# Kernel tuning notes

Hardware: AMD Instinct MI355X
Metric: run time of the kernel (lower is better)

The kernel has to match this reference:

```python
import jax, jax.numpy as jnp
import numpy as np

NUM_GRAPHS = 1024
NODES_PER_GRAPH = 128
NUM_EDGES = 1048576
D_IN = 128          # n_heads * head_out_feats = input/concat dim
ATT_HEADS = 2       # intra/inter GATConv(d, 32, 2) as in HDN-DDI repo
ATT_OUT = 32
POOL_HEADS = 2      # pool = GATConv(128, 64, 2)
POOL_OUT = 64
EPS = 1e-5          # PyG LayerNorm eps


def _segment_softmax(e, seg, n):
    # numerically-stable softmax over edges grouped by destination node
    m = jax.ops.segment_max(e, seg, num_segments=n)
    m = jnp.where(jnp.isfinite(m), m, 0.0)
    p = jnp.exp(e - m[seg])
    s = jax.ops.segment_sum(p, seg, num_segments=n)
    return p / (s[seg] + 1e-16)


def _gat(x_src, x_dst, edge_index, w_src, w_dst, att_src, att_dst, bias, self_loops):
    # PyG GATConv: linear -> per-head attention logits -> leaky_relu(0.2) ->
    # softmax over incoming edges -> weighted sum of source features -> concat heads + bias
    H, C = att_src.shape
    nd = x_dst.shape[0]
    hs = (x_src @ w_src).reshape(-1, H, C)   # [Ns,H,C]
    hd = (x_dst @ w_dst).reshape(-1, H, C)   # [Nd,H,C]
    a_s = jnp.einsum('nhc,hc->nh', hs, att_src)
    a_d = jnp.einsum('nhc,hc->nh', hd, att_dst)
    src, dst = edge_index[0], edge_index[1]
    if self_loops:  # PyG default add_self_loops=True (non-bipartite case)
        loop = jnp.arange(nd)
        src = jnp.concatenate([src, loop])
        dst = jnp.concatenate([dst, loop])
    e = jax.nn.leaky_relu(a_s[src] + a_d[dst], 0.2)  # [E,H]
    alpha = _segment_softmax(e, dst, nd)
    out = jax.ops.segment_sum(hs[src] * alpha[:, :, None], dst, num_segments=nd)
    return out.reshape(nd, H * C) + bias


def _graph_layernorm(x, batch, weight, bias, n_graphs):
    # PyG LayerNorm(mode='graph'): normalize over all nodes+channels of each graph
    f = x.shape[-1]
    cnt = jax.ops.segment_sum(jnp.ones((x.shape[0],), x.dtype), batch, num_segments=n_graphs)
    norm = jnp.maximum(cnt, 1.0) * f
    mean = jax.ops.segment_sum(x.sum(-1), batch, num_segments=n_graphs) / norm
    xc = x - mean[batch][:, None]
    var = jax.ops.segment_sum((xc * xc).sum(-1), batch, num_segments=n_graphs) / norm
    return (xc / jnp.sqrt(var + EPS)[batch][:, None]) * weight + bias


def setup_inputs() -> dict:
    key = jax.random.key(0)
    ks = jax.random.split(key, 24)
    B, P, E, D = NUM_GRAPHS, NODES_PER_GRAPH, NUM_EDGES, D_IN
    N = B * P

    def intra_edges(k):  # within-graph edges, no self-loops
        k1, k2, k3 = jax.random.split(k, 3)
        g = jax.random.randint(k1, (E,), 0, B)
        s = jax.random.randint(k2, (E,), 0, P)
        d = (s + 1 + jax.random.randint(k3, (E,), 0, P - 1)) % P
        return jnp.stack([g * P + s, g * P + d])

    def inter_edges(k):  # bipartite head-node -> tail-node edges within same graph pair
        k1, k2, k3 = jax.random.split(k, 3)
        g = jax.random.randint(k1, (E,), 0, B)
        s = jax.random.randint(k2, (E,), 0, P)
        d = jax.random.randint(k3, (E,), 0, P)
        return jnp.stack([g * P + s, g * P + d])

    batch = jnp.repeat(jnp.arange(B), P)
    # one global supernode (type 2) per graph: the last node
    y = jnp.tile(jnp.concatenate([jnp.zeros((P - 1,), jnp.int32), jnp.array([2], jnp.int32)]), B)
    p = lambda k, shape: jax.random.normal(k, shape, jnp.float32) * 0.1
    return {
        'h_x': jax.random.normal(ks[0], (N, D), jnp.float32),
        't_x': jax.random.normal(ks[1], (N, D), jnp.float32),
        'h_edge_index': intra_edges(ks[2]),
        't_edge_index': intra_edges(ks[3]),
        'b_edge_index': inter_edges(ks[4]),
        'h_batch': batch,
        't_batch': batch,
        'h_y': y,
        't_y': y,
        'w_intra': p(ks[5], (D, ATT_HEADS * ATT_OUT)),
        'att_intra_src': p(ks[6], (ATT_HEADS, ATT_OUT)),
        'att_intra_dst': p(ks[7], (ATT_HEADS, ATT_OUT)),
        'b_intra': jnp.zeros((ATT_HEADS * ATT_OUT,), jnp.float32),
        'w_inter_src': p(ks[8], (D, ATT_HEADS * ATT_OUT)),
        'w_inter_dst': p(ks[9], (D, ATT_HEADS * ATT_OUT)),
        'att_inter_src': p(ks[10], (ATT_HEADS, ATT_OUT)),
        'att_inter_dst': p(ks[11], (ATT_HEADS, ATT_OUT)),
        'b_inter': jnp.zeros((ATT_HEADS * ATT_OUT,), jnp.float32),
        'w_pool': p(ks[12], (D, POOL_HEADS * POOL_OUT)),
        'att_pool_src': p(ks[13], (POOL_HEADS, POOL_OUT)),
        'att_pool_dst': p(ks[14], (POOL_HEADS, POOL_OUT)),
        'b_pool': jnp.zeros((POOL_HEADS * POOL_OUT,), jnp.float32),
        'ln_weight': jnp.ones((D,), jnp.float32),
        'ln_bias': jnp.zeros((D,), jnp.float32),
    }


def reference(h_x, t_x, h_edge_index, t_edge_index, b_edge_index, h_batch, t_batch, h_y, t_y,
              w_intra, att_intra_src, att_intra_dst, b_intra,
              w_inter_src, w_inter_dst, att_inter_src, att_inter_dst, b_inter,
              w_pool, att_pool_src, att_pool_dst, b_pool, ln_weight, ln_bias):
    h_in = jax.nn.elu(h_x)
    t_in = jax.nn.elu(t_x)
    # intra-graph attention (shared GATConv applied to both drug graphs)
    h_intra = _gat(h_in, h_in, h_edge_index, w_intra, w_intra, att_intra_src, att_intra_dst, b_intra, True)
    t_intra = _gat(t_in, t_in, t_edge_index, w_intra, w_intra, att_intra_src, att_intra_dst, b_intra, True)
    # inter-graph (bipartite) attention: h->t and reversed t->h with shared weights
    t_inter = _gat(h_in, t_in, b_edge_index, w_inter_src, w_inter_dst, att_inter_src, att_inter_dst, b_inter, False)
    h_inter = _gat(t_in, h_in, b_edge_index[::-1], w_inter_src, w_inter_dst, att_inter_src, att_inter_dst, b_inter, False)
    h_rep = jnp.concatenate([h_intra, h_inter], 1)  # [N, 128]
    t_rep = jnp.concatenate([t_intra, t_inter], 1)
    h_nx = jax.nn.elu(_graph_layernorm(h_rep, h_batch, ln_weight, ln_bias, NUM_GRAPHS))
    t_nx = jax.nn.elu(_graph_layernorm(t_rep, t_batch, ln_weight, ln_bias, NUM_GRAPHS))
    h_out = _gat(h_nx, h_nx, h_edge_index, w_pool, w_pool, att_pool_src, att_pool_dst, b_pool, True)
    t_out = _gat(t_nx, t_nx, t_edge_index, w_pool, w_pool, att_pool_src, att_pool_dst, b_pool, True)
    # get_node: gather the single type-2 supernode per graph (exactly NUM_GRAPHS of them)
    h_idx = jnp.where(h_y == 2, size=NUM_GRAPHS)[0]
    t_idx = jnp.where(t_y == 2, size=NUM_GRAPHS)[0]
    return h_out, t_out, h_out[h_idx], t_out[t_idx]
```

## Files before the change

### kernel.cpp

```cpp
#include <hip/hip_runtime.h>
#include <hip/hip_bf16.h>

#define NN 131072
#define NG 1024
#define NE 1048576
#define EB 16384
#define NB 64
#define EMAX 1536

typedef __hip_bfloat16 bf16;
typedef __attribute__((ext_vector_type(8))) short short8v;
typedef __attribute__((ext_vector_type(4))) float f32x4;

__device__ __forceinline__ float b2f(bf16 v){ return __bfloat162float(v); }
__device__ __forceinline__ bf16 f2b(float v){ return __float2bfloat16(v); }
__device__ __forceinline__ unsigned short f2bu(float v){ bf16 b = f2b(v); return *(unsigned short*)&b; }
__device__ __forceinline__ float eluf(float x){ return x > 0.f ? x : expm1f(x); }
__device__ __forceinline__ float lrelu(float x){ return x >= 0.f ? x : 0.2f*x; }

__device__ __forceinline__ float ldx(const void* p, size_t i, int f){
  return f ? ((const float*)p)[i] : b2f(((const bf16*)p)[i]);
}

struct EPtrs { const int *s0,*d0,*s1,*d1,*s2,*d2,*s3,*d3; };

__global__ void detect_dtype(const unsigned short* __restrict__ x, int* __restrict__ flag){
  if (blockIdx.x==0 && threadIdx.x==0){
    int bad = 0;
    for (int i=0;i<2048;i++){
      unsigned short e = (x[i] >> 7) & 0xFF;
      if (e == 0xFF) bad++;
      else if (e >= 0x90) bad++;
      else if (e != 0 && e < 0x60) bad++;
    }
    *flag = (bad > 64) ? 1 : 0;
  }
}

__global__ __launch_bounds__(256) void hist_bagg(EPtrs ep, int* __restrict__ Hb){
  __shared__ int cnt[NG];
  int set = blockIdx.y, blk = blockIdx.x, t = threadIdx.x;
  const int* dp = set==0 ? ep.d0 : set==1 ? ep.d1 : set==2 ? ep.d2 : ep.d3;
  for (int i=t;i<NG;i+=256) cnt[i]=0;
  __syncthreads();
  int e0 = blk*EB;
  for (int i=t;i<EB;i+=256) atomicAdd(&cnt[dp[e0+i]>>7],1);
  __syncthreads();
  for (int i=t;i<NG;i+=256) Hb[((size_t)set*NB+blk)*NG+i] = cnt[i];
}

__global__ __launch_bounds__(1024) void scan_bagg(const int* __restrict__ Hb, int* __restrict__ Bb,
                                                  int* __restrict__ base_gs){
  __shared__ int sh[1024];
  int set = blockIdx.x, t = threadIdx.x;
  int run = 0;
  for (int b=0;b<NB;b++){
    int v = Hb[((size_t)set*NB + b)*NG + t];
    Bb[((size_t)set*NB + b)*NG + t] = run;
    run += v;
  }
  int val = run; sh[t] = run; __syncthreads();
  for (int d=1; d<1024; d<<=1){
    int add = (t>=d)? sh[t-d] : 0; __syncthreads();
    val += add; sh[t] = val; __syncthreads();
  }
  int binbase = val - run;
  base_gs[set*(NG+1) + t] = binbase;
  if (t==1023) base_gs[set*(NG+1)+NG] = val;
  for (int b=0;b<NB;b++) Bb[((size_t)set*NB + b)*NG + t] += binbase;
}

__global__ __launch_bounds__(256) void scatter_bagg(EPtrs ep, const int* __restrict__ Bb,
                                                    unsigned short* __restrict__ pk){
  __shared__ int cur[NG];
  int set = blockIdx.y, blk = blockIdx.x, t = threadIdx.x;
  const int* sp = set==0 ? ep.s0 : set==1 ? ep.s1 : set==2 ? ep.s2 : ep.s3;
  const int* dp = set==0 ? ep.d0 : set==1 ? ep.d1 : set==2 ? ep.d2 : ep.d3;
  for (int i=t;i<NG;i+=256) cur[i] = Bb[((size_t)set*NB+blk)*NG+i];
  __syncthreads();
  int e0 = blk*EB;
  for (int i=t;i<EB;i+=256){
    int e = e0+i;
    int d = dp[e], s = sp[e];
    int p = atomicAdd(&cur[d>>7],1);
    pk[(size_t)set*NE + p] = (unsigned short)(((d & 127) << 8) | (s & 127));
  }
}

__global__ __launch_bounds__(256) void build_csr(const unsigned short* __restrict__ pk, const int* __restrict__ base,
                                                 unsigned char* __restrict__ srcs8, int* __restrict__ offs4){
  __shared__ int hist[128], excl[128], cur[128];
  __shared__ unsigned char ob[8192];
  int set = blockIdx.y, g = blockIdx.x, t = threadIdx.x;
  int n0 = base[set*(NG+1) + g], n1 = base[set*(NG+1) + g + 1];
  int cnt = min(n1 - n0, 8192);
  if (t < 128) hist[t] = 0;
  __syncthreads();
  const unsigned short* PK = pk + (size_t)set*NE + n0;
  for (int i=t; i<cnt; i+=256) atomicAdd(&hist[PK[i]>>8], 1);
  __syncthreads();
  if (t < 128) excl[t] = hist[t];
  __syncthreads();
  for (int d=1; d<128; d<<=1){
    int v = (t < 128 && t >= d) ? excl[t-d] : 0;
    __syncthreads();
    if (t < 128) excl[t] += v;
    __syncthreads();
  }
  if (t < 128){
    int e_ = excl[t] - hist[t];
    cur[t] = e_;
    offs4[(size_t)set*(NN+1) + g*128 + t] = n0 + e_;
  }
  if (g == NG-1 && t == 0) offs4[(size_t)set*(NN+1) + NN] = NE;
  __syncthreads();
  for (int i=t; i<cnt; i+=256){
    unsigned short v = PK[i];
    int p = atomicAdd(&cur[v>>8], 1);
    ob[p] = (unsigned char)(v & 127);
  }
  __syncthreads();
  unsigned char* S = srcs8 + (size_t)set*NE + n0;
  for (int i=t; i<cnt; i+=256) S[i] = ob[i];
}

__global__ __launch_bounds__(256) void prep_kernel(
    const void* w_intra, const void* w_isrc, const void* w_idst, const void* att_xd, const void* w_pool,
    const void* att_is, const void* att_id, const void* att_xs,
    const void* att_ps, const void* att_pd,
    const void* b_intra, const void* b_inter, const void* b_pool,
    const void* ln_w, const void* ln_b,
    bf16* __restrict__ Wtc, bf16* __restrict__ Wtp, float* __restrict__ vdst, float* __restrict__ sm,
    const int* __restrict__ fp){
  int f = *fp;
  int t = threadIdx.x;
  for (int i=t; i<16384; i+=256){
    int j = i & 7, l = (i>>3) & 63, ks = (i>>9) & 3, nt = i >> 11;
    int k = ks*32 + ((l>>4)<<3) + j;
    int c = nt*16 + (l & 15);
    float w1 = (c < 64) ? ldx(w_intra, k*64 + c, f) : ldx(w_isrc, k*64 + (c-64), f);
    Wtc[i] = f2b(w1);
    Wtp[i] = f2b(ldx(w_pool, k*128 + c, f));
  }
  {
    int k = t>>1, h = t&1; float a = 0.f;
    for (int c=0;c<32;c++) a += ldx(w_idst, k*64 + h*32 + c, f) * ldx(att_xd, h*32 + c, f);
    vdst[t] = a;
  }
  if (t < 64){
    sm[t]     = ldx(att_is, t, f);
    sm[64+t]  = ldx(att_id, t, f);
    sm[128+t] = ldx(att_xs, t, f);
    sm[448+t] = ldx(b_intra, t, f);
    sm[512+t] = ldx(b_inter, t, f);
  }
  if (t < 128){
    sm[192+t] = ldx(att_ps, t, f);
    sm[320+t] = ldx(att_pd, t, f);
    sm[576+t] = ldx(b_pool, t, f);
    sm[704+t] = ldx(ln_w, t, f);
    sm[832+t] = ldx(ln_b, t, f);
  }
}

template<int MODE>
__global__ __launch_bounds__(256) void gemm_fused(const void* A, const bf16* __restrict__ Wt, bf16* __restrict__ C,
    const int* __restrict__ fp, const int* __restrict__ fsel, size_t aoff_bf, size_t aoff_f32,
    const float* __restrict__ vdst,
    const float* __restrict__ attA, const float* __restrict__ attB, const float* __restrict__ attC,
    float* __restrict__ oS, float* __restrict__ oD, float* __restrict__ oX, float* __restrict__ oDx){
  constexpr bool ELU = (MODE==0);
  const bf16* Ab = (const bf16*)A + ((fp == nullptr && fsel && *fsel) ? aoff_f32 : aoff_bf);
  int tid = threadIdx.x;
  int w = tid >> 6, l = tid & 63;
  int lr = l & 15, lg = l >> 4;
  size_t row = (size_t)blockIdx.x*64 + w*16 + lr;
  int f = fp ? *fp : 0;
  f32x4 acc[8];
  #pragma unroll
  for (int nt=0;nt<8;nt++) acc[nt] = (f32x4){0.f,0.f,0.f,0.f};
  float dx0 = 0.f, dx1 = 0.f;
  #pragma unroll
  for (int ks=0;ks<4;ks++){
    short8v af;
    size_t ab = row*128 + ks*32 + lg*8;
    if (fp){
      if (f){
        const float* Af = (const float*)A;
        #pragma unroll
        for (int j=0;j<8;j++){
          float v = Af[ab+j]; if (ELU) v = eluf(v);
          if constexpr (MODE==0){ int k = ks*32+lg*8+j; dx0 += v*vdst[k*2]; dx1 += v*vdst[k*2+1]; }
          ((unsigned short*)&af)[j] = f2bu(v);
        }
      } else {
        const unsigned short* Au = (const unsigned short*)A;
        short8v raw = *(const short8v*)(Au + ab);
        #pragma unroll
        for (int j=0;j<8;j++){
          bf16 b; *(unsigned short*)&b = ((unsigned short*)&raw)[j];
          float v = b2f(b); if (ELU) v = eluf(v);
          if constexpr (MODE==0){ int k = ks*32+lg*8+j; dx0 += v*vdst[k*2]; dx1 += v*vdst[k*2+1]; }
          ((unsigned short*)&af)[j] = f2bu(v);
        }
      }
    } else {
      af = *(const short8v*)((const unsigned short*)Ab + ab);
    }
    #pragma unroll
    for (int nt=0;nt<8;nt++){
      short8v bfr = *(const short8v*)((const unsigned short*)Wt + (size_t)((nt*4+ks)*64 + l)*8);
      acc[nt] = __builtin_amdgcn_mfma_f32_16x16x32_bf16(af, bfr, acc[nt], 0, 0, 0);
    }
  }
  if constexpr (MODE==0){
    dx0 += __shfl_xor(dx0, 16); dx0 += __shfl_xor(dx0, 32);
    dx1 += __shfl_xor(dx1, 16); dx1 += __shfl_xor(dx1, 32);
    if (lg == 0){ oDx[row*2] = dx0; oDx[row*2+1] = dx1; }
  }
  size_t crow = (size_t)blockIdx.x*64 + w*16 + lg*4;
  #pragma unroll
  for (int nt=0;nt<8;nt++)
    #pragma unroll
    for (int r=0;r<4;r++)
      C[(crow + r)*128 + nt*16 + lr] = f2b(acc[nt][r]);
  #pragma unroll
  for (int rg=0; rg<4; ++rg){
    float pS0=0.f,pS1=0.f,pD0=0.f,pD1=0.f,pX0=0.f,pX1=0.f;
    #pragma unroll
    for (int nt=0;nt<8;nt++){
      float v = acc[nt][rg];
      int c = nt*16 + lr;
      if constexpr (MODE==0){
        if (nt<4){
          float a=attA[c], b=attB[c];
          if (nt<2){ pS0+=v*a; pD0+=v*b; } else { pS1+=v*a; pD1+=v*b; }
        } else {
          float xw=attC[c-64];
          if (nt<6) pX0+=v*xw; else pX1+=v*xw;
        }
      } else {
        float a=attA[c], b=attB[c];
        if (nt<4){ pS0+=v*a; pD0+=v*b; } else { pS1+=v*a; pD1+=v*b; }
      }
    }
    #pragma unroll
    for (int o=1;o<16;o<<=1){
      pS0+=__shfl_xor(pS0,o); pS1+=__shfl_xor(pS1,o);
      pD0+=__shfl_xor(pD0,o); pD1+=__shfl_xor(pD1,o);
      if constexpr (MODE==0){ pX0+=__shfl_xor(pX0,o); pX1+=__shfl_xor(pX1,o); }
    }
    if (lr == 0){
      size_t n = crow + rg;
      oS[n*2]=pS0; oS[n*2+1]=pS1;
      oD[n*2]=pD0; oD[n*2+1]=pD1;
      if constexpr (MODE==0){ oX[n*2]=pX0; oX[n*2+1]=pX1; }
    }
  }
}

struct GatSet {
  const int* offs;
  const unsigned char* srcs;
  const bf16* F;
  const float* aS;
  const float* aD;
  const float* bias;
  int col_in;
  int self_loops;
  int col_off;
  int pad;
  size_t obase_bf, obase_f32, gbase;
};
struct GatSet4 { GatSet s[4]; };

template<int FD>
__global__ __launch_bounds__(512) void gat_mfma(GatSet4 sets, void* out,
    const int* __restrict__ fp, const int* __restrict__ fsel){
  constexpr int NH = FD/2;
  constexpr int NT = NH/16;
  constexpr int KSH = (FD==64)?5:6;
  __shared__ bf16 Ft[NH*136];
  __shared__ bf16 Pm[128*136];
  __shared__ float2 aSs[128];
  __shared__ float rsum[128];
  __shared__ unsigned char ss[EMAX];
  __shared__ int begs[129];
  const GatSet S = sets.s[blockIdx.y];
  int fo = fp ? *fp : -1;
  size_t obase = (fsel && *fsel) ? S.obase_f32 : S.obase_bf;
  int g = blockIdx.x, t = threadIdx.x;

  if (t < 129) begs[t] = S.offs[g*128 + t];
  if (t >= 256 && t < 384) aSs[t-256] = ((const float2*)S.aS)[g*128 + (t-256)];
  __syncthreads();
  int gbeg = begs[0];
  int Eg = min(begs[128] - gbeg, EMAX);
  int w = t >> 6, l = t & 63, lr = l & 15, lg = l >> 4;

  #pragma unroll
  for (int h=0; h<2; ++h){
    for (int i=t; i<128*68; i+=512) ((unsigned int*)Pm)[i] = 0;
    if (h==0) for (int i=t; i<Eg; i+=512) ss[i] = S.srcs[gbeg + i];
    __syncthreads();
    if (t < 128){
      int r = t;
      float ad = S.aD[(size_t)(g*128+r)*2 + h];
      int b = begs[r]-gbeg, e = min(begs[r+1]-gbeg, EMAX);
      float rs = 0.f;
      unsigned short* Pr = (unsigned short*)Pm + r*136;
      for (int j=b; j<e; ++j){
        int s = ss[j];
        float2 as2 = aSs[s];
        float p = __expf(lrelu((h ? as2.y : as2.x) + ad));
        bf16 ov; *(unsigned short*)&ov = Pr[s];
        Pr[s] = f2bu(b2f(ov) + p);
        rs += p;
      }
      if (S.self_loops){
        float2 as2 = aSs[r];
        float p = __expf(lrelu((h ? as2.y : as2.x) + ad));
        bf16 ov; *(unsigned short*)&ov = Pr[r];
        Pr[r] = f2bu(b2f(ov) + p);
        rs += p;
      }
      rsum[r] = rs;
    } else {
      const unsigned short* Fu = (const unsigned short*)S.F;
      unsigned short* FtU = (unsigned short*)Ft;
      int ft = t - 128;
      for (int i=ft; i<NH*128; i+=384){
        int c = i & (NH-1), k = i >> KSH;
        FtU[c*136 + k] = Fu[((size_t)(g*128+k))*128 + S.col_in + h*NH + c];
      }
    }
    __syncthreads();
    f32x4 acc[NT];
    #pragma unroll
    for (int nt=0;nt<NT;nt++) acc[nt] = (f32x4){0.f,0.f,0.f,0.f};
    #pragma unroll
    for (int ks=0;ks<4;ks++){
      short8v af = *(const short8v*)((const unsigned short*)Pm + (w*16+lr)*136 + ks*32 + lg*8);
      #pragma unroll
      for (int nt=0;nt<NT;nt++){
        short8v bfr = *(const short8v*)((const unsigned short*)Ft + (nt*16 + lr)*136 + ks*32 + lg*8);
        acc[nt] = __builtin_amdgcn_mfma_f32_16x16x32_bf16(af, bfr, acc[nt], 0, 0, 0);
      }
    }
    #pragma unroll
    for (int rg=0; rg<4; ++rg){
      int rrow = w*16 + lg*4 + rg;
      float rinv = 1.f / (rsum[rrow] + 1e-16f);
      int n = g*128 + rrow;
      bool gw = (fp != nullptr) && (rrow == 127);
      #pragma unroll
      for (int nt=0;nt<NT;nt++){
        int c = h*NH + nt*16 + lr;
        float o = acc[nt][rg]*rinv + S.bias[c];
        size_t oi = obase + (size_t)n*128 + S.col_off + c;
        if (fo > 0){
          ((float*)out)[oi] = o;
          if (gw) ((float*)out)[S.gbase + (size_t)g*128 + c] = o;
        } else {
          ((bf16*)out)[oi] = f2b(o);
          if (gw) ((bf16*)out)[S.gbase + (size_t)g*128 + c] = f2b(o);
        }
      }
    }
    __syncthreads();
  }
}

__global__ __launch_bounds__(512) void graph_ln_m(bf16* R_, size_t off_t_bf, size_t off_t_f32,
    const int* __restrict__ fsel, const float* __restrict__ wv, const float* __restrict__ bv){
  __shared__ float sh1[8], sh2[8];
  int g = blockIdx.x, t = threadIdx.x;
  int side = g >> 10, gl = g & 1023;
  size_t soff = side ? ((*fsel) ? off_t_f32 : off_t_bf) : 0;
  unsigned short* Ru = (unsigned short*)(R_ + soff + (size_t)gl*16384);
  short8v v[4];
  #pragma unroll
  for (int q=0;q<4;q++) v[q] = *(short8v*)(Ru + q*4096 + t*8);
  float s1=0.f, s2=0.f;
  #pragma unroll
  for (int q=0;q<4;q++)
    #pragma unroll
    for (int j=0;j<8;j++){
      bf16 b; *(unsigned short*)&b = ((unsigned short*)&v[q])[j];
      float x = b2f(b); s1 += x; s2 += x*x;
    }
  #pragma unroll
  for (int o=32;o;o>>=1){ s1 += __shfl_xor(s1,o); s2 += __shfl_xor(s2,o); }
  if ((t&63)==0){ sh1[t>>6]=s1; sh2[t>>6]=s2; }
  __syncthreads();
  float S1=0.f,S2=0.f;
  #pragma unroll
  for (int i=0;i<8;i++){ S1+=sh1[i]; S2+=sh2[i]; }
  float mean = S1 * (1.f/16384.f);
  float var = fmaxf(S2*(1.f/16384.f) - mean*mean, 0.f);
  float rstd = rsqrtf(var + 1e-5f);
  #pragma unroll
  for (int q=0;q<4;q++){
    short8v ov;
    #pragma unroll
    for (int j=0;j<8;j++){
      int c = (t*8 + j) & 127;
      bf16 b; *(unsigned short*)&b = ((unsigned short*)&v[q])[j];
      float y = (b2f(b)-mean)*rstd*wv[c] + bv[c];
      ((unsigned short*)&ov)[j] = f2bu(y>0.f ? y : expm1f(y));
    }
    *(short8v*)(Ru + q*4096 + t*8) = ov;
  }
}

extern "C" void kernel_launch(void* const* d_in, const int* in_sizes, int n_in,
                              void* d_out, int out_size, void* d_ws, size_t ws_size,
                              hipStream_t stream){
  (void)in_sizes; (void)n_in; (void)out_size; (void)ws_size;
  const void* h_x = d_in[0];
  const void* t_x = d_in[1];
  const int* h_ei = (const int*)d_in[2];
  const int* t_ei = (const int*)d_in[3];
  const int* b_ei = (const int*)d_in[4];

  char* base = (char*)d_ws;
  size_t off = 0;
  auto alloc = [&](size_t bytes)->char*{ char* p = base + off; off += (bytes + 255) & ~(size_t)255; return p; };
  bf16* AB_h     = (bf16*)alloc((size_t)NN*128*2);
  bf16* AB_t     = (bf16*)alloc((size_t)NN*128*2);
  unsigned short* pk = (unsigned short*)alloc((size_t)4*NE*2);
  unsigned char* srcs8 = (unsigned char*)alloc((size_t)4*NE);
  int* offs4     = (int*)alloc((size_t)4*(NN+1)*4);
  int* Hb        = (int*)alloc((size_t)4*NB*NG*4);
  int* Bb        = (int*)alloc((size_t)4*NB*NG*4);
  int* base_gs   = (int*)alloc((size_t)4*(NG+1)*4);
  float* aSi_h   = (float*)alloc((size_t)NN*2*4);
  float* aDi_h   = (float*)alloc((size_t)NN*2*4);
  float* aSx_h   = (float*)alloc((size_t)NN*2*4);
  float* aSi_t   = (float*)alloc((size_t)NN*2*4);
  float* aDi_t   = (float*)alloc((size_t)NN*2*4);
  float* aSx_t   = (float*)alloc((size_t)NN*2*4);
  float* aDx_h   = (float*)alloc((size_t)NN*2*4);
  float* aDx_t   = (float*)alloc((size_t)NN*2*4);
  bf16* Wtc      = (bf16*)alloc(16384*2);
  bf16* Wtp      = (bf16*)alloc(16384*2);
  float* vdst    = (float*)alloc(256*4);
  float* sm      = (float*)alloc(960*4);
  int* flag      = (int*)alloc(256);

  const size_t REPT_BF = (size_t)NN*128, REPT_F32 = (size_t)2*NN*128;

  detect_dtype<<<1,64,0,stream>>>((const unsigned short*)h_x, flag);

  EPtrs ep;
  ep.s0 = h_ei;      ep.d0 = h_ei + NE;
  ep.s1 = t_ei;      ep.d1 = t_ei + NE;
  ep.s2 = b_ei;      ep.d2 = b_ei + NE;
  ep.s3 = b_ei + NE; ep.d3 = b_ei;
  hist_bagg<<<dim3(NB,4),256,0,stream>>>(ep, Hb);
  scan_bagg<<<4,1024,0,stream>>>(Hb, Bb, base_gs);
  scatter_bagg<<<dim3(NB,4),256,0,stream>>>(ep, Bb, pk);
  build_csr<<<dim3(NG,4),256,0,stream>>>(pk, base_gs, srcs8, offs4);

  prep_kernel<<<1,256,0,stream>>>(d_in[9], d_in[13], d_in[14], d_in[16], d_in[18],
      d_in[10], d_in[11], d_in[15], d_in[19], d_in[20],
      d_in[12], d_in[17], d_in[21], d_in[22], d_in[23],
      Wtc, Wtp, vdst, sm, flag);

  const int* offs_h = offs4;
  const int* offs_t = offs4 + (NN+1);
  const int* offs_ht= offs4 + 2*(NN+1);
  const int* offs_th= offs4 + 3*(NN+1);
  const unsigned char* srcs_h = srcs8;
  const unsigned char* srcs_t = srcs8 + NE;
  const unsigned char* srcs_ht= srcs8 + (size_t)2*NE;
  const unsigned char* srcs_th= srcs8 + (size_t)3*NE;

  gemm_fused<0><<<2048,256,0,stream>>>(h_x, Wtc, AB_h, flag, nullptr, 0, 0,
      vdst, sm+0, sm+64, sm+128, aSi_h, aDi_h, aSx_h, aDx_h);
  gemm_fused<0><<<2048,256,0,stream>>>(t_x, Wtc, AB_t, flag, nullptr, 0, 0,
      vdst, sm+0, sm+64, sm+128, aSi_t, aDi_t, aSx_t, aDx_t);

  {
    GatSet4 L;
    L.s[0] = { offs_h,  srcs_h,  AB_h, aSi_h, aDi_h, sm+448, 0,  1, 0,  0, 0,        0,         0 };
    L.s[1] = { offs_t,  srcs_t,  AB_t, aSi_t, aDi_t, sm+448, 0,  1, 0,  0, REPT_BF,  REPT_F32,  0 };
    L.s[2] = { offs_ht, srcs_ht, AB_h, aSx_h, aDx_t, sm+512, 64, 0, 64, 0, REPT_BF,  REPT_F32,  0 };
    L.s[3] = { offs_th, srcs_th, AB_t, aSx_t, aDx_h, sm+512, 64, 0, 64, 0, 0,        0,         0 };
    gat_mfma<64><<<dim3(NG,4),512,0,stream>>>(L, d_out, nullptr, flag);
  }

  graph_ln_m<<<2048,512,0,stream>>>((bf16*)d_out, REPT_BF, REPT_F32, flag, sm+704, sm+832);

  gemm_fused<1><<<2048,256,0,stream>>>(d_out, Wtp, AB_h, nullptr, flag, 0, 0,
      nullptr, sm+192, sm+320, nullptr, aSi_h, aDi_h, nullptr, nullptr);
  gemm_fused<1><<<2048,256,0,stream>>>(d_out, Wtp, AB_t, nullptr, flag, REPT_BF, REPT_F32,
      nullptr, sm+192, sm+320, nullptr, aSi_t, aDi_t, nullptr, nullptr);

  {
    size_t gb_h = (size_t)2*NN*128;
    size_t gb_t = gb_h + (size_t)NG*128;
    GatSet4 P;
    P.s[0] = { offs_h, srcs_h, AB_h, aSi_h, aDi_h, sm+576, 0, 1, 0, 0, 0,              0,              gb_h };
    P.s[1] = { offs_t, srcs_t, AB_t, aSi_t, aDi_t, sm+576, 0, 1, 0, 0, (size_t)NN*128, (size_t)NN*128, gb_t };
    P.s[2] = P.s[0]; P.s[3] = P.s[0];
    gat_mfma<128><<<dim3(NG,2),512,0,stream>>>(P, d_out, flag, flag);
  }
}
```

Measured before the change: 615.5 us.

## Replace per-graph CSR build with in-block packed edge multiplicity matrix

Drops the build_csr kernel and instead has each GAT block scatter packed (dst,src) edges into a shared-memory 128x128 matrix of 4-bit multiplicity counters via atomics. Attention weights are then computed densely for all 128 sources per row by four threads in parallel, instead of one thread serially walking each row's edge list. Shared tiles switch from padding to XOR swizzling, and the feature tile load is no longer overlapped with the softmax pass. This removes one kernel launch and its global memory traffic, plus the serial per-row loop, at the cost of dense exp work and a risk of counter overflow for highly duplicated edges.

```diff
diff --git a/kernel.cpp b/kernel.cpp
--- a/kernel.cpp
+++ b/kernel.cpp
@@ -6,7 +6,6 @@
 #define NE 1048576
 #define EB 16384
 #define NB 64
-#define EMAX 1536
 
 typedef __hip_bfloat16 bf16;
 typedef __attribute__((ext_vector_type(8))) short short8v;
@@ -85,43 +84,6 @@
     int p = atomicAdd(&cur[d>>7],1);
     pk[(size_t)set*NE + p] = (unsigned short)(((d & 127) << 8) | (s & 127));
   }
-}
-
-__global__ __launch_bounds__(256) void build_csr(const unsigned short* __restrict__ pk, const int* __restrict__ base,
-                                                 unsigned char* __restrict__ srcs8, int* __restrict__ offs4){
-  __shared__ int hist[128], excl[128], cur[128];
-  __shared__ unsigned char ob[8192];
-  int set = blockIdx.y, g = blockIdx.x, t = threadIdx.x;
-  int n0 = base[set*(NG+1) + g], n1 = base[set*(NG+1) + g + 1];
-  int cnt = min(n1 - n0, 8192);
-  if (t < 128) hist[t] = 0;
-  __syncthreads();
-  const unsigned short* PK = pk + (size_t)set*NE + n0;
-  for (int i=t; i<cnt; i+=256) atomicAdd(&hist[PK[i]>>8], 1);
-  __syncthreads();
-  if (t < 128) excl[t] = hist[t];
-  __syncthreads();
-  for (int d=1; d<128; d<<=1){
-    int v = (t < 128 && t >= d) ? excl[t-d] : 0;
-    __syncthreads();
-    if (t < 128) excl[t] += v;
-    __syncthreads();
-  }
-  if (t < 128){
-    int e_ = excl[t] - hist[t];
-    cur[t] = e_;
-    offs4[(size_t)set*(NN+1) + g*128 + t] = n0 + e_;
-  }
-  if (g == NG-1 && t == 0) offs4[(size_t)set*(NN+1) + NN] = NE;
-  __syncthreads();
-  for (int i=t; i<cnt; i+=256){
-    unsigned short v = PK[i];
-    int p = atomicAdd(&cur[v>>8], 1);
-    ob[p] = (unsigned char)(v & 127);
-  }
-  __syncthreads();
-  unsigned char* S = srcs8 + (size_t)set*NE + n0;
-  for (int i=t; i<cnt; i+=256) S[i] = ob[i];
 }
 
 __global__ __launch_bounds__(256) void prep_kernel(
@@ -260,8 +222,8 @@
 }
 
 struct GatSet {
-  const int* offs;
-  const unsigned char* srcs;
+  const unsigned short* pk;
+  const int* gb;
   const bf16* F;
   const float* aS;
   const float* aD;
@@ -280,70 +242,89 @@
   constexpr int NH = FD/2;
   constexpr int NT = NH/16;
   constexpr int KSH = (FD==64)?5:6;
-  __shared__ bf16 Ft[NH*136];
-  __shared__ bf16 Pm[128*136];
-  __shared__ float2 aSs[128];
-  __shared__ float rsum[128];
-  __shared__ unsigned char ss[EMAX];
-  __shared__ int begs[129];
+  __shared__ bf16 Pm[128*128];
+  __shared__ bf16 Ft[NH*128];
+  __shared__ unsigned int Msh[128*16];
+  __shared__ float aS0[128], aS1[128], aD0[128], aD1[128], rsum[128];
   const GatSet S = sets.s[blockIdx.y];
   int fo = fp ? *fp : -1;
   size_t obase = (fsel && *fsel) ? S.obase_f32 : S.obase_bf;
   int g = blockIdx.x, t = threadIdx.x;
 
-  if (t < 129) begs[t] = S.offs[g*128 + t];
-  if (t >= 256 && t < 384) aSs[t-256] = ((const float2*)S.aS)[g*128 + (t-256)];
-  __syncthreads();
-  int gbeg = begs[0];
-  int Eg = min(begs[128] - gbeg, EMAX);
+  if (t < 128){
+    float2 v = ((const float2*)S.aS)[g*128+t]; aS0[t]=v.x; aS1[t]=v.y;
+    float2 d = ((const float2*)S.aD)[g*128+t]; aD0[t]=d.x; aD1[t]=d.y;
+  }
+  for (int i=t;i<2048;i+=512) Msh[i]=0;
+  __syncthreads();
+
+  {
+    int gbeg = S.gb[g], gend = S.gb[g+1];
+    for (int i=gbeg+t; i<gend; i+=512){
+      unsigned v = S.pk[i];
+      unsigned r = v>>8, s = v&127;
+      atomicAdd(&Msh[r*16 + (s>>3)], 1u<<((s&7)*4));
+    }
+    if (S.self_loops && t<128) atomicAdd(&Msh[t*16 + (t>>3)], 1u<<((t&7)*4));
+  }
+  {
+    const unsigned short* Fu = (const unsigned short*)S.F;
+    unsigned short* FtU = (unsigned short*)Ft;
+    for (int i=t; i<NH*128; i+=512){
+      int c = i & (NH-1), k = i >> KSH;
+      FtU[c*128 + (k ^ (8*(c&7)))] = Fu[((size_t)(g*128+k))*128 + S.col_in + c];
+    }
+  }
+  __syncthreads();
+
   int w = t >> 6, l = t & 63, lr = l & 15, lg = l >> 4;
+  int r = t >> 2, q = t & 3;
 
   #pragma unroll
   for (int h=0; h<2; ++h){
-    for (int i=t; i<128*68; i+=512) ((unsigned int*)Pm)[i] = 0;
-    if (h==0) for (int i=t; i<Eg; i+=512) ss[i] = S.srcs[gbeg + i];
-    __syncthreads();
-    if (t < 128){
-      int r = t;
-      float ad = S.aD[(size_t)(g*128+r)*2 + h];
-      int b = begs[r]-gbeg, e = min(begs[r+1]-gbeg, EMAX);
-      float rs = 0.f;
-      unsigned short* Pr = (unsigned short*)Pm + r*136;
-      for (int j=b; j<e; ++j){
-        int s = ss[j];
-        float2 as2 = aSs[s];
-        float p = __expf(lrelu((h ? as2.y : as2.x) + ad));
-        bf16 ov; *(unsigned short*)&ov = Pr[s];
-        Pr[s] = f2bu(b2f(ov) + p);
-        rs += p;
-      }
-      if (S.self_loops){
-        float2 as2 = aSs[r];
-        float p = __expf(lrelu((h ? as2.y : as2.x) + ad));
-        bf16 ov; *(unsigned short*)&ov = Pr[r];
-        Pr[r] = f2bu(b2f(ov) + p);
-        rs += p;
-      }
-      rsum[r] = rs;
-    } else {
+    if (h == 1){
       const unsigned short* Fu = (const unsigned short*)S.F;
       unsigned short* FtU = (unsigned short*)Ft;
-      int ft = t - 128;
-      for (int i=ft; i<NH*128; i+=384){
+      for (int i=t; i<NH*128; i+=512){
         int c = i & (NH-1), k = i >> KSH;
-        FtU[c*136 + k] = Fu[((size_t)(g*128+k))*128 + S.col_in + h*NH + c];
-      }
+        FtU[c*128 + (k ^ (8*(c&7)))] = Fu[((size_t)(g*128+k))*128 + S.col_in + NH + c];
+      }
+    }
+    {
+      float ad = h ? aD1[r] : aD0[r];
+      const float* aSh = h ? aS1 : aS0;
+      float rs = 0.f;
+      unsigned int* PmW = (unsigned int*)Pm;
+      int dbase = r*64, sw = 4*(r&7);
+      unsigned mw = 0;
+      #pragma unroll
+      for (int i=0;i<16;i++){
+        int c = q*32 + 2*i;
+        if ((i&3)==0) mw = Msh[r*16 + (c>>3)];
+        float m0 = (float)((mw >> ((c&7)*4)) & 15u);
+        float m1 = (float)((mw >> (((c&7)+1)*4)) & 15u);
+        float p0 = m0 * __expf(lrelu(aSh[c]   + ad));
+        float p1 = m1 * __expf(lrelu(aSh[c+1] + ad));
+        rs += p0 + p1;
+        PmW[dbase + ((q*16+i) ^ sw)] = (unsigned)f2bu(p0) | ((unsigned)f2bu(p1)<<16);
+      }
+      rs += __shfl_xor(rs,1); rs += __shfl_xor(rs,2);
+      if (q==0) rsum[r] = rs;
     }
     __syncthreads();
     f32x4 acc[NT];
     #pragma unroll
     for (int nt=0;nt<NT;nt++) acc[nt] = (f32x4){0.f,0.f,0.f,0.f};
+    const unsigned short* PmU = (const unsigned short*)Pm;
+    const unsigned short* FtU = (const unsigned short*)Ft;
+    int arow = w*16 + lr;
     #pragma unroll
     for (int ks=0;ks<4;ks++){
-      short8v af = *(const short8v*)((const unsigned short*)Pm + (w*16+lr)*136 + ks*32 + lg*8);
+      short8v af = *(const short8v*)(PmU + arow*128 + ((ks*32+lg*8) ^ (8*(arow&7))));
       #pragma unroll
       for (int nt=0;nt<NT;nt++){
-        short8v bfr = *(const short8v*)((const unsigned short*)Ft + (nt*16 + lr)*136 + ks*32 + lg*8);
+        int brow = nt*16 + lr;
+        short8v bfr = *(const short8v*)(FtU + brow*128 + ((ks*32+lg*8) ^ (8*(brow&7))));
         acc[nt] = __builtin_amdgcn_mfma_f32_16x16x32_bf16(af, bfr, acc[nt], 0, 0, 0);
       }
     }
@@ -429,8 +410,6 @@
   bf16* AB_h     = (bf16*)alloc((size_t)NN*128*2);
   bf16* AB_t     = (bf16*)alloc((size_t)NN*128*2);
   unsigned short* pk = (unsigned short*)alloc((size_t)4*NE*2);
-  unsigned char* srcs8 = (unsigned char*)alloc((size_t)4*NE);
-  int* offs4     = (int*)alloc((size_t)4*(NN+1)*4);
   int* Hb        = (int*)alloc((size_t)4*NB*NG*4);
   int* Bb        = (int*)alloc((size_t)4*NB*NG*4);
   int* base_gs   = (int*)alloc((size_t)4*(NG+1)*4);
@@ -460,21 +439,20 @@
   hist_bagg<<<dim3(NB,4),256,0,stream>>>(ep, Hb);
   scan_bagg<<<4,1024,0,stream>>>(Hb, Bb, base_gs);
   scatter_bagg<<<dim3(NB,4),256,0,stream>>>(ep, Bb, pk);
-  build_csr<<<dim3(NG,4),256,0,stream>>>(pk, base_gs, srcs8, offs4);
 
   prep_kernel<<<1,256,0,stream>>>(d_in[9], d_in[13], d_in[14], d_in[16], d_in[18],
       d_in[10], d_in[11], d_in[15], d_in[19], d_in[20],
       d_in[12], d_in[17], d_in[21], d_in[22], d_in[23],
       Wtc, Wtp, vdst, sm, flag);
 
-  const int* offs_h = offs4;
-  const int* offs_t = offs4 + (NN+1);
-  const int* offs_ht= offs4 + 2*(NN+1);
-  const int* offs_th= offs4 + 3*(NN+1);
-  const unsigned char* srcs_h = srcs8;
-  const unsigned char* srcs_t = srcs8 + NE;
-  const unsigned char* srcs_ht= srcs8 + (size_t)2*NE;
-  const unsigned char* srcs_th= srcs8 + (size_t)3*NE;
+  const unsigned short* pk_h = pk;
+  const unsigned short* pk_t = pk + NE;
+  const unsigned short* pk_ht= pk + (size_t)2*NE;
+  const unsigned short* pk_th= pk + (size_t)3*NE;
+  const int* gb_h = base_gs;
+  const int* gb_t = base_gs + (NG+1);
+  const int* gb_ht= base_gs + 2*(NG+1);
+  const int* gb_th= base_gs + 3*(NG+1);
 
   gemm_fused<0><<<2048,256,0,stream>>>(h_x, Wtc, AB_h, flag, nullptr, 0, 0,
       vdst, sm+0, sm+64, sm+128, aSi_h, aDi_h, aSx_h, aDx_h);
@@ -483,10 +461,10 @@
 
   {
     GatSet4 L;
-    L.s[0] = { offs_h,  srcs_h,  AB_h, aSi_h, aDi_h, sm+448, 0,  1, 0,  0, 0,        0,         0 };
-    L.s[1] = { offs_t,  srcs_t,  AB_t, aSi_t, aDi_t, sm+448, 0,  1, 0,  0, REPT_BF,  REPT_F32,  0 };
-    L.s[2] = { offs_ht, srcs_ht, AB_h, aSx_h, aDx_t, sm+512, 64, 0, 64, 0, REPT_BF,  REPT_F32,  0 };
-    L.s[3] = { offs_th, srcs_th, AB_t, aSx_t, aDx_h, sm+512, 64, 0, 64, 0, 0,        0,         0 };
+    L.s[0] = { pk_h,  gb_h,  AB_h, aSi_h, aDi_h, sm+448, 0,  1, 0,  0, 0,        0,         0 };
+    L.s[1] = { pk_t,  gb_t,  AB_t, aSi_t, aDi_t, sm+448, 0,  1, 0,  0, REPT_BF,  REPT_F32,  0 };
+    L.s[2] = { pk_ht, gb_ht, AB_h, aSx_h, aDx_t, sm+512, 64, 0, 64, 0, REPT_BF,  REPT_F32,  0 };
+    L.s[3] = { pk_th, gb_th, AB_t, aSx_t, aDx_h, sm+512, 64, 0, 64, 0, 0,        0,         0 };
     gat_mfma<64><<<dim3(NG,4),512,0,stream>>>(L, d_out, nullptr, flag);
   }
 
@@ -498,11 +476,11 @@
       nullptr, sm+192, sm+320, nullptr, aSi_t, aDi_t, nullptr, nullptr);
 
   {
-    size_t gb_h = (size_t)2*NN*128;
-    size_t gb_t = gb_h + (size_t)NG*128;
+    size_t go_h = (size_t)2*NN*128;
+    size_t go_t = go_h + (size_t)NG*128;
     GatSet4 P;
-    P.s[0] = { offs_h, srcs_h, AB_h, aSi_h, aDi_h, sm+576, 0, 1, 0, 0, 0,              0,              gb_h };
-    P.s[1] = { offs_t, srcs_t, AB_t, aSi_t, aDi_t, sm+576, 0, 1, 0, 0, (size_t)NN*128, (size_t)NN*128, gb_t };
+    P.s[0] = { pk_h, gb_h, AB_h, aSi_h, aDi_h, sm+576, 0, 1, 0, 0, 0,              0,              go_h };
+    P.s[1] = { pk_t, gb_t, AB_t, aSi_t, aDi_t, sm+576, 0, 1, 0, 0, (size_t)NN*128, (size_t)NN*128, go_t };
     P.s[2] = P.s[0]; P.s[3] = P.s[0];
     gat_mfma<128><<<dim3(NG,2),512,0,stream>>>(P, d_out, flag, flag);
   }
```

New measurement: 629.7 us. 2.3% more time.
